# Kernel tuning notes

Hardware: AMD Instinct MI355X
Metric: run time of the kernel (lower is better)

## Reference

```python
import jax, jax.numpy as jnp
import numpy as np

H = 128
N_EXPERT = 100000
N_TEAM = 50000
N_EDGE = 600000
N_LABEL = 500000


def _sage(x_src, x_dst, src, dst, Wl, Wr, b, n_dst):
    # PyG SAGEConv: lin_l(mean of gathered neighbor feats) + lin_r(x_dst)
    msg = x_src[src]                                   # [E, H] gather
    agg = jax.ops.segment_sum(msg, dst, num_segments=n_dst)      # [n_dst, H]
    cnt = jax.ops.segment_sum(jnp.ones((src.shape[0], 1), x_src.dtype), dst,
                              num_segments=n_dst)      # [n_dst, 1]
    agg = agg / jnp.maximum(cnt, 1.0)
    return agg @ Wl + b + x_dst @ Wr


def setup_inputs() -> dict:
    key = jax.random.key(0)
    ks = jax.random.split(key, 20)
    inp = {
        'x_expert': jax.random.normal(ks[0], (N_EXPERT, H), jnp.float32),
        'x_team': jax.random.normal(ks[1], (N_TEAM, H), jnp.float32),
        'src_expert': jax.random.randint(ks[2], (N_EDGE,), 0, N_EXPERT),
        'dst_team': jax.random.randint(ks[3], (N_EDGE,), 0, N_TEAM),
        'label_src': jax.random.randint(ks[4], (N_LABEL,), 0, N_EXPERT),
        'label_dst': jax.random.randint(ks[5], (N_LABEL,), 0, N_TEAM),
    }
    s = 0.02
    names = ['W1et_l', 'W1et_r', 'W1te_l', 'W1te_r',
             'W2et_l', 'W2et_r', 'W2te_l', 'W2te_r']
    for i, n in enumerate(names):
        inp[n] = s * jax.random.normal(ks[6 + i], (H, H), jnp.float32)
    for i, n in enumerate(['b1et', 'b1te', 'b2et', 'b2te']):
        inp[n] = jnp.zeros((H,), jnp.float32)
    return inp


def reference(x_expert, x_team, src_expert, dst_team, label_src, label_dst,
              W1et_l, W1et_r, W1te_l, W1te_r,
              W2et_l, W2et_r, W2te_l, W2te_r,
              b1et, b1te, b2et, b2te):
    n_e, n_t = x_expert.shape[0], x_team.shape[0]
    # layer 1 (hetero: expert->team and reverse team->expert), ReLU
    h_team = jax.nn.relu(_sage(x_expert, x_team, src_expert, dst_team,
                               W1et_l, W1et_r, b1et, n_t))
    h_expert = jax.nn.relu(_sage(x_team, x_expert, dst_team, src_expert,
                                 W1te_l, W1te_r, b1te, n_e))
    # layer 2, no activation
    z_team = _sage(h_expert, h_team, src_expert, dst_team,
                   W2et_l, W2et_r, b2et, n_t)
    z_expert = _sage(h_team, h_expert, dst_team, src_expert,
                     W2te_l, W2te_r, b2te, n_e)
    # edge dot-product classifier on supervision edges
    return (z_expert[label_src] * z_team[label_dst]).sum(axis=-1)
```

## Files before the change

kernel.cpp:

```cpp
#include <hip/hip_runtime.h>

#define H 128
#define CH 4096
typedef unsigned short ushort_t;
typedef unsigned int uint_t;
typedef unsigned long long u64_t;
using s16x8 = __attribute__((ext_vector_type(8))) short;
using f32x4 = __attribute__((ext_vector_type(4))) float;
using h2 = __attribute__((ext_vector_type(2))) _Float16;

__device__ __forceinline__ float dot2(uint_t a, uint_t b, float c) {
  return __builtin_amdgcn_fdot2(__builtin_bit_cast(h2, a), __builtin_bit_cast(h2, b), c, false);
}
__device__ __forceinline__ uint_t pkh(float a, float b) {
  return __builtin_bit_cast(uint_t, __builtin_amdgcn_cvt_pkrtz(a, b));
}

__device__ __forceinline__ void gload_lds16(const void* g, void* l) {
  __builtin_amdgcn_global_load_lds(
      (const __attribute__((address_space(1))) unsigned int*)(unsigned long long)g,
      (__attribute__((address_space(3))) unsigned int*)(unsigned int)(unsigned long long)l,
      16, 0, 0);
}

__global__ __launch_bounds__(256) void prep_kernel(
    const float* __restrict__ xa, const float* __restrict__ xb,
    size_t n4a, size_t n4tot, uint2* __restrict__ xout,
    const float* __restrict__ Wl0, const float* __restrict__ Wr0,
    const float* __restrict__ Wl1, const float* __restrict__ Wr1,
    const float* __restrict__ Wl2, const float* __restrict__ Wr2,
    const float* __restrict__ Wl3, const float* __restrict__ Wr3,
    ushort_t* __restrict__ wdst, int* __restrict__ bcnt, int nbz) {
  const int b = blockIdx.x;
  const int tid = threadIdx.x;
  if (b < 2048) {
    size_t i = (size_t)b * 256 + tid;
    size_t s = 2048 * 256;
    for (; i < n4tot; i += s) {
      float4 v = (i < n4a) ? ((const float4*)xa)[i] : ((const float4*)xb)[i - n4a];
      uint2 r;
      r.x = pkh(v.x, v.y);
      r.y = pkh(v.z, v.w);
      xout[i] = r;
    }
  } else if (b < 2560) {
    int i = (b - 2048) * 256 + tid;
    int w = i >> 15;
    int ii = i & 32767;
    int j = ii & 7;
    int lane = (ii >> 3) & 63;
    int nf = (ii >> 9) & 7;
    int ks = ii >> 12;
    int k = ks * 32 + (lane >> 4) * 8 + j;
    int nn = nf * 16 + (lane & 15);
    const float* Wl = (w == 0) ? Wl0 : (w == 1) ? Wl1 : (w == 2) ? Wl2 : Wl3;
    const float* Wr = (w == 0) ? Wr0 : (w == 1) ? Wr1 : (w == 2) ? Wr2 : Wr3;
    float v = (k < H) ? Wl[k * H + nn] : Wr[(k - H) * H + nn];
    wdst[i] = __builtin_bit_cast(ushort_t, (_Float16)v);
  } else {
    for (int i = tid; i < nbz; i += 256) bcnt[i] = 0;
  }
}

__global__ __launch_bounds__(256) void bucket_count(
    const int* __restrict__ src, const int* __restrict__ dst, const int* __restrict__ ld,
    int* __restrict__ bcnt, int E, int L, int nct, int NBt, int NBe) {
  __shared__ int hist[256];
  const int b = blockIdx.x;
  const int tid = threadIdx.x;
  int stream, i0, n, base, shift;
  if (b < nct) { stream = 0; i0 = b * CH; n = E; base = 0; shift = 8; }
  else if (b < 2 * nct) { stream = 1; i0 = (b - nct) * CH; n = E; base = NBt; shift = 9; }
  else { stream = 2; i0 = (b - 2 * nct) * CH; n = L; base = NBt + NBe; shift = 8; }
  const int* idx = (stream == 0) ? dst : (stream == 1) ? src : ld;
  const int i1 = min(n, i0 + CH);
  hist[tid] = 0;
  __syncthreads();
  for (int i = i0 + tid; i < i1; i += 256) atomicAdd(&hist[idx[i] >> shift], 1);
  __syncthreads();
  int h = hist[tid];
  if (h) atomicAdd(&bcnt[base + tid], h);
}

__global__ void scan_buckets(const int* __restrict__ bcnt, int* __restrict__ boff,
                             int* __restrict__ cur, int n) {
  __shared__ int s[256];
  const int t = threadIdx.x;
  int carry = 0;
  for (int base = 0; base < n; base += 256) {
    int i = base + t;
    int v = (i < n) ? bcnt[i] : 0;
    s[t] = v;
    __syncthreads();
    for (int off = 1; off < 256; off <<= 1) {
      int x = (t >= off) ? s[t - off] : 0;
      __syncthreads();
      s[t] += x;
      __syncthreads();
    }
    if (i < n) { boff[i] = s[t] - v + carry; cur[i] = s[t] - v + carry; }
    __syncthreads();
    carry += s[255];
    __syncthreads();
  }
  if (t == 0) boff[n] = carry;
}

__global__ __launch_bounds__(256) void bucket_scatter(
    const int* __restrict__ src, const int* __restrict__ dst,
    const int* __restrict__ ls, const int* __restrict__ ld,
    int* __restrict__ cur, u64_t* __restrict__ recs,
    int E, int L, int nct, int NBt, int NBe) {
  __shared__ int hist[256];
  __shared__ int start[256];
  const int b = blockIdx.x;
  const int tid = threadIdx.x;
  int stream, i0, n, base;
  if (b < nct) { stream = 0; i0 = b * CH; n = E; base = 0; }
  else if (b < 2 * nct) { stream = 1; i0 = (b - nct) * CH; n = E; base = NBt; }
  else { stream = 2; i0 = (b - 2 * nct) * CH; n = L; base = NBt + NBe; }
  const int i1 = min(n, i0 + CH);

  hist[tid] = 0;
  __syncthreads();
  for (int i = i0 + tid; i < i1; i += 256) {
    int d = (stream == 0) ? dst[i] : (stream == 1) ? src[i] : ld[i];
    int bkt = (stream == 1) ? (d >> 9) : (d >> 8);
    atomicAdd(&hist[bkt], 1);
  }
  __syncthreads();
  int h = hist[tid];
  if (h) start[tid] = atomicAdd(&cur[base + tid], h);
  __syncthreads();
  for (int i = i0 + tid; i < i1; i += 256) {
    u64_t rec;
    int bkt;
    if (stream == 0) {
      int d = dst[i];
      rec = ((u64_t)d << 32) | (uint_t)src[i];
      bkt = d >> 8;
    } else if (stream == 1) {
      int d = src[i];
      rec = ((u64_t)d << 32) | (uint_t)dst[i];
      bkt = d >> 9;
    } else {
      int d = ld[i];
      rec = ((u64_t)d << 40) | ((u64_t)(uint_t)ls[i] << 20) | (uint_t)i;
      bkt = d >> 8;
    }
    int pos = start[bkt] + atomicSub(&hist[bkt], 1) - 1;
    recs[pos] = rec;
  }
}

__global__ __launch_bounds__(256) void place_all(
    const u64_t* __restrict__ recs, const int* __restrict__ boff,
    int* __restrict__ off_t, int* __restrict__ off_e, int* __restrict__ off_l,
    int* __restrict__ adj_t, int* __restrict__ adj_e_m, long long* __restrict__ lpair_m,
    int n_t, int n_e, int NBt, int NBe, int NBl) {
  __shared__ int sh[512];
  __shared__ int tmp[256];
  const int b = blockIdx.x;
  const int tid = threadIdx.x;
  int stream, d0, d1, nmax;
  int* offg;
  if (b < NBt) { stream = 0; d0 = b << 8; d1 = min(n_t, d0 + 256); offg = off_t; nmax = n_t; }
  else if (b < NBt + NBe) { stream = 1; d0 = (b - NBt) << 9; d1 = min(n_e, d0 + 512); offg = off_e; nmax = n_e; }
  else { stream = 2; d0 = (b - NBt - NBe) << 8; d1 = min(n_t, d0 + 256); offg = off_l; nmax = n_t; }
  const int nn = d1 - d0;
  const int rs = boff[b], re = boff[b + 1];

  sh[tid] = 0;
  sh[tid + 256] = 0;
  __syncthreads();
  for (int i = rs + tid; i < re; i += 256) {
    u64_t rec = recs[i];
    int d = (stream == 2) ? (int)(rec >> 40) : (int)(rec >> 32);
    atomicAdd(&sh[d - d0], 1);
  }
  __syncthreads();
  int carry = 0;
  for (int c = 0; c < 2; ++c) {
    int idx = c * 256 + tid;
    int v = sh[idx];
    tmp[tid] = v;
    __syncthreads();
    for (int o = 1; o < 256; o <<= 1) {
      int x = (tid >= o) ? tmp[tid - o] : 0;
      __syncthreads();
      tmp[tid] += x;
      __syncthreads();
    }
    int excl = tmp[tid] - v + carry;
    if (idx < nn) {
      offg[d0 + idx] = rs + excl;
      sh[idx] = rs + excl;
    }
    __syncthreads();
    carry += tmp[255];
    __syncthreads();
  }
  if (tid == 0) {
    bool last = (stream == 0 && b == NBt - 1) ||
                (stream == 1 && b == NBt + NBe - 1) ||
                (stream == 2 && b == NBt + NBe + NBl - 1);
    if (last) offg[nmax] = re;
  }
  __syncthreads();
  if (stream == 0) {
    for (int i = rs + tid; i < re; i += 256) {
      u64_t rec = recs[i];
      int d = (int)(rec >> 32);
      adj_t[atomicAdd(&sh[d - d0], 1)] = (int)rec;
    }
  } else if (stream == 1) {
    for (int i = rs + tid; i < re; i += 256) {
      u64_t rec = recs[i];
      int d = (int)(rec >> 32);
      adj_e_m[atomicAdd(&sh[d - d0], 1)] = (int)rec;
    }
  } else {
    for (int i = rs + tid; i < re; i += 256) {
      u64_t rec = recs[i];
      int d = (int)(rec >> 40);
      int lsv = (int)((rec >> 20) & 0xFFFFF);
      int li = (int)(rec & 0xFFFFF);
      lpair_m[atomicAdd(&sh[d - d0], 1)] = ((long long)lsv << 32) | (uint_t)li;
    }
  }
}

__global__ void pull_mean_dual(
    const ushort_t* __restrict__ featA, const int* __restrict__ offA, const int* __restrict__ adjA,
    ushort_t* __restrict__ outA, int nA,
    const ushort_t* __restrict__ featB, const int* __restrict__ offB, const int* __restrict__ adjB,
    ushort_t* __restrict__ outB, int nB) {
  int gid = blockIdx.x * blockDim.x + threadIdx.x;
  int wave = gid >> 6;
  int lane = gid & 63;
  int slot = lane >> 4;
  int sl = lane & 15;
  int nw = (gridDim.x * blockDim.x) >> 6;
  for (int v = wave; v < nA + nB; v += nw) {
    const uint4* f;
    const int* off;
    const int* adj;
    uint4* o;
    int vv;
    if (v < nA) {
      f = (const uint4*)featA; off = offA; adj = adjA; o = (uint4*)outA; vv = v;
    } else {
      f = (const uint4*)featB; off = offB; adj = adjB; o = (uint4*)outB; vv = v - nA;
    }
    int s = off[vv], e = off[vv + 1];
    float acc[8];
#pragma unroll
    for (int c = 0; c < 8; ++c) acc[c] = 0.f;
#pragma unroll 2
    for (int i = s; i < e; i += 4) {
      int j = i + slot;
      bool val = j < e;
      int idx = adj[val ? j : i];
      uint4 u = f[(size_t)idx * 16 + sl];
      uint_t s_lo = val ? 0x00003C00u : 0u;
      uint_t s_hi = val ? 0x3C000000u : 0u;
      acc[0] = dot2(u.x, s_lo, acc[0]); acc[1] = dot2(u.x, s_hi, acc[1]);
      acc[2] = dot2(u.y, s_lo, acc[2]); acc[3] = dot2(u.y, s_hi, acc[3]);
      acc[4] = dot2(u.z, s_lo, acc[4]); acc[5] = dot2(u.z, s_hi, acc[5]);
      acc[6] = dot2(u.w, s_lo, acc[6]); acc[7] = dot2(u.w, s_hi, acc[7]);
    }
#pragma unroll
    for (int c = 0; c < 8; ++c) {
      acc[c] += __shfl_xor(acc[c], 16);
      acc[c] += __shfl_xor(acc[c], 32);
    }
    if (slot == 0) {
      float rd = 1.0f / fmaxf((float)(e - s), 1.0f);
      uint4 ov;
      ov.x = pkh(acc[0] * rd, acc[1] * rd);
      ov.y = pkh(acc[2] * rd, acc[3] * rd);
      ov.z = pkh(acc[4] * rd, acc[5] * rd);
      ov.w = pkh(acc[6] * rd, acc[7] * rd);
      o[(size_t)vv * 16 + sl] = ov;
    }
  }
}

template <bool RELU>
__global__ __launch_bounds__(256, 2) void gemm_mfma_dual(
    const ushort_t* __restrict__ aggA, const ushort_t* __restrict__ xdA,
    const ushort_t* __restrict__ wfA, const float* __restrict__ biasA,
    ushort_t* __restrict__ outA, int nA, int gA,
    const ushort_t* __restrict__ aggB, const ushort_t* __restrict__ xdB,
    const ushort_t* __restrict__ wfB, const float* __restrict__ biasB,
    ushort_t* __restrict__ outB, int nB) {
  __shared__ __align__(16) ushort_t sA[64 * 128];
  __shared__ __align__(16) ushort_t sX[64 * 128];
  const ushort_t *agg, *xd, *wfrag;
  const float* bias;
  ushort_t* outp;
  int n, b0, nbl;
  if ((int)blockIdx.x < gA) {
    agg = aggA; xd = xdA; wfrag = wfA; bias = biasA; outp = outA; n = nA;
    b0 = blockIdx.x; nbl = gA;
  } else {
    agg = aggB; xd = xdB; wfrag = wfB; bias = biasB; outp = outB; n = nB;
    b0 = blockIdx.x - gA; nbl = gridDim.x - gA;
  }
  const int t = threadIdx.x;
  const int lane = t & 63;
  const int wid = t >> 6;
  const int mrow = (wid >> 1) * 32;
  const int nhalf = (wid & 1) * 64;

  s16x8 B[8][4];
#pragma unroll
  for (int ks = 0; ks < 8; ++ks)
#pragma unroll
    for (int nfi = 0; nfi < 4; ++nfi)
      B[ks][nfi] = *(const s16x8*)(wfrag + (size_t)(((ks << 3) | ((nhalf >> 4) + nfi)) << 9) + (lane << 3));

  float bv[4];
#pragma unroll
  for (int nfi = 0; nfi < 4; ++nfi) bv[nfi] = bias[nhalf + nfi * 16 + (lane & 15)];

  const int lrow = lane >> 4;
  const int pbyte = (lane & 15) << 4;

  const int ntiles = (n + 63) >> 6;
  for (int tile = b0; tile < ntiles; tile += nbl) {
    const int row0 = tile << 6;
#pragma unroll
    for (int i = 0; i < 8; ++i) {
      int reg = (wid << 3) + i;
      int rr = ((reg & 15) << 2) + lrow;
      int row = row0 + rr;
      row = row < n ? row : n - 1;
      int pp = pbyte ^ ((rr & 7) << 4);
      const ushort_t* srcp = (reg < 16 ? agg : xd) + (size_t)row * H + (pp >> 1);
      ushort_t* ldst = (reg < 16 ? sA : sX) + ((reg & 15) << 9);
      gload_lds16(srcp, ldst);
    }
    __syncthreads();

    f32x4 acc[2][4];
#pragma unroll
    for (int mi = 0; mi < 2; ++mi)
#pragma unroll
      for (int nfi = 0; nfi < 4; ++nfi) {
        f32x4 c = {bv[nfi], bv[nfi], bv[nfi], bv[nfi]};
        acc[mi][nfi] = c;
      }

    const int rr0 = mrow + (lane & 15);
    const int rr1 = rr0 + 16;
    const int kx = (lane >> 4) << 4;
    const int sw = (rr0 & 7) << 4;
#pragma unroll
    for (int ks = 0; ks < 8; ++ks) {
      const ushort_t* base = (ks < 4) ? sA : sX;
      const int kb = (ks & 3) << 6;
      s16x8 a0 = *(const s16x8*)((const char*)base + rr0 * 256 + ((kb | kx) ^ sw));
      s16x8 a1 = *(const s16x8*)((const char*)base + rr1 * 256 + ((kb | kx) ^ sw));
#pragma unroll
      for (int nfi = 0; nfi < 4; ++nfi) {
        acc[0][nfi] = __builtin_amdgcn_mfma_f32_16x16x32_f16(a0, B[ks][nfi], acc[0][nfi], 0, 0, 0);
        acc[1][nfi] = __builtin_amdgcn_mfma_f32_16x16x32_f16(a1, B[ks][nfi], acc[1][nfi], 0, 0, 0);
      }
    }

#pragma unroll
    for (int mi = 0; mi < 2; ++mi) {
      int rbase = row0 + mrow + mi * 16 + ((lane >> 4) << 2);
#pragma unroll
      for (int r = 0; r < 4; ++r) {
        int row = rbase + r;
        if (row < n) {
#pragma unroll
          for (int nfi = 0; nfi < 4; ++nfi) {
            float v = acc[mi][nfi][r];
            if (RELU) v = fmaxf(v, 0.f);
            outp[(size_t)row * H + nhalf + nfi * 16 + (lane & 15)] =
                __builtin_bit_cast(ushort_t, (_Float16)v);
          }
        }
      }
    }
    __syncthreads();
  }
}

__global__ void edge_dot_grouped(const ushort_t* __restrict__ ze, const ushort_t* __restrict__ zt,
                                 const int* __restrict__ loff, const long long* __restrict__ lpair,
                                 float* __restrict__ out, int n_t) {
  int gid = blockIdx.x * blockDim.x + threadIdx.x;
  int wave = gid >> 6;
  int lane = gid & 63;
  int slot = lane >> 4;
  int sl = lane & 15;
  int nw = (gridDim.x * blockDim.x) >> 6;
  const uint4* fz = (const uint4*)ze;
  const uint4* ft = (const uint4*)zt;
  for (int v = wave; v < n_t; v += nw) {
    int s = loff[v], e = loff[v + 1];
    if (s == e) continue;
    uint4 b = ft[(size_t)v * 16 + sl];
    for (int i = s; i < e; i += 4) {
      int j = i + slot;
      bool val = j < e;
      long long q = lpair[val ? j : i];
      int row = (int)(q >> 32);
      uint4 u = fz[(size_t)row * 16 + sl];
      float p = dot2(u.x, b.x, dot2(u.y, b.y, dot2(u.z, b.z, dot2(u.w, b.w, 0.f))));
      p += __shfl_xor(p, 1);
      p += __shfl_xor(p, 2);
      p += __shfl_xor(p, 4);
      p += __shfl_xor(p, 8);
      if (sl == 0 && val) __builtin_nontemporal_store(p, &out[(int)q]);
    }
  }
}

extern "C" void kernel_launch(void* const* d_in, const int* in_sizes, int n_in,
                              void* d_out, int out_size, void* d_ws, size_t ws_size,
                              hipStream_t stream) {
  const float* x_e = (const float*)d_in[0];
  const float* x_t = (const float*)d_in[1];
  const int* src = (const int*)d_in[2];
  const int* dst = (const int*)d_in[3];
  const int* ls = (const int*)d_in[4];
  const int* ld = (const int*)d_in[5];
  const float* W1et_l = (const float*)d_in[6];
  const float* W1et_r = (const float*)d_in[7];
  const float* W1te_l = (const float*)d_in[8];
  const float* W1te_r = (const float*)d_in[9];
  const float* W2et_l = (const float*)d_in[10];
  const float* W2et_r = (const float*)d_in[11];
  const float* W2te_l = (const float*)d_in[12];
  const float* W2te_r = (const float*)d_in[13];
  const float* b1et = (const float*)d_in[14];
  const float* b1te = (const float*)d_in[15];
  const float* b2et = (const float*)d_in[16];
  const float* b2te = (const float*)d_in[17];

  const int n_e = in_sizes[0] / H;
  const int n_t = in_sizes[1] / H;
  const int E = in_sizes[2];
  const int L = in_sizes[4];
  float* out = (float*)d_out;

  const size_t fe = (size_t)n_e * H;
  const size_t ft = (size_t)n_t * H;
  ushort_t* us = (ushort_t*)d_ws;
  ushort_t* xb_e = us;
  ushort_t* xb_t = xb_e + fe;
  ushort_t* agg_e = xb_t + ft;
  ushort_t* agg_t = agg_e + fe;
  ushort_t* h_e = agg_t + ft;
  ushort_t* h_t = h_e + fe;
  ushort_t* wfrag = h_t + ft;
  int* ib = (int*)(wfrag + 4 * 32768);

  const int Mt = n_t + 1, Me = n_e + 1, Ml = n_t + 1;
  const int NBt = (n_t + 255) >> 8;
  const int NBe = (n_e + 511) >> 9;
  const int NBl = NBt;
  const int NBtot = NBt + NBe + NBl;

  int* off = ib;
  int* bcnt = off + Mt + Me + Ml;
  int* boff = bcnt + NBtot + 1;
  int* cur = boff + NBtot + 1;
  int* adj_t = cur + NBtot;
  int* adj_e = adj_t + E;
  long long* lpair = (long long*)(((unsigned long long)(adj_e + E) + 7) & ~7ULL);
  u64_t* recs = (u64_t*)(lpair + L);

  int* off_t = off;
  int* off_e = off + Mt;
  int* off_l = off + Mt + Me;
  int* adj_e_m = adj_e - E;
  long long* lpair_m = lpair - 2 * (size_t)E;

  const int nct = (E + CH - 1) / CH;
  const int ncl = (L + CH - 1) / CH;

  const dim3 blk(256);

  prep_kernel<<<2561, blk, 0, stream>>>(x_e, x_t, fe / 4, (fe + ft) / 4, (uint2*)xb_e,
                                        W1et_l, W1et_r, W1te_l, W1te_r,
                                        W2et_l, W2et_r, W2te_l, W2te_r,
                                        wfrag, bcnt, NBtot + 1);

  bucket_count<<<2 * nct + ncl, blk, 0, stream>>>(src, dst, ld, bcnt, E, L, nct, NBt, NBe);
  scan_buckets<<<1, blk, 0, stream>>>(bcnt, boff, cur, NBtot);
  bucket_scatter<<<2 * nct + ncl, blk, 0, stream>>>(src, dst, ls, ld, cur, recs,
                                                    E, L, nct, NBt, NBe);
  place_all<<<NBtot, blk, 0, stream>>>(recs, boff, off_t, off_e, off_l,
                                       adj_t, adj_e_m, lpair_m, n_t, n_e, NBt, NBe, NBl);

  const int gt = (n_t + 63) / 64, ge = (n_e + 63) / 64;
  const int gA = min(gt, 512), gB = min(ge, 512);
  const int npull = ((n_t + n_e) + 3) / 4;

  pull_mean_dual<<<npull, blk, 0, stream>>>(xb_e, off_t, adj_t, agg_t, n_t,
                                            xb_t, off_e, adj_e_m, agg_e, n_e);
  gemm_mfma_dual<true><<<gA + gB, blk, 0, stream>>>(
      agg_t, xb_t, wfrag + 0 * 32768, b1et, h_t, n_t, gA,
      agg_e, xb_e, wfrag + 1 * 32768, b1te, h_e, n_e);

  pull_mean_dual<<<npull, blk, 0, stream>>>(h_e, off_t, adj_t, agg_t, n_t,
                                            h_t, off_e, adj_e_m, agg_e, n_e);
  gemm_mfma_dual<false><<<gA + gB, blk, 0, stream>>>(
      agg_t, h_t, wfrag + 2 * 32768, b2et, agg_t, n_t, gA,
      agg_e, h_e, wfrag + 3 * 32768, b2te, agg_e, n_e);

  edge_dot_grouped<<<(n_t + 3) / 4, blk, 0, stream>>>(agg_e, agg_t, off_l, lpair_m, out, n_t);
}
```

Measured before the change: 250.7 us.

## Fuse bucket counting into prep, regroup labels by expert, vectorize adjacency reads

The bucket histogram pass is folded into the prep kernel as extra blocks, and the zeroing of bucket counters moves to a memset. This removes one kernel launch. Supervision edges are now grouped by expert (label_src) instead of team, so each wave holds an expert row and gathers team rows, which come from a smaller table. The pull-mean and edge-dot loops now give each 16-lane slot four consecutive edges, with int4 loads of adjacency indices. That can leave lanes idle on low-degree nodes, and the int4 loads may be unaligned.

```diff
diff --git a/kernel.cpp b/kernel.cpp
--- a/kernel.cpp
+++ b/kernel.cpp
@@ -15,6 +15,8 @@
 __device__ __forceinline__ uint_t pkh(float a, float b) {
   return __builtin_bit_cast(uint_t, __builtin_amdgcn_cvt_pkrtz(a, b));
 }
+#define LO1 0x00003C00u
+#define HI1 0x3C000000u
 
 __device__ __forceinline__ void gload_lds16(const void* g, void* l) {
   __builtin_amdgcn_global_load_lds(
@@ -30,7 +32,9 @@
     const float* __restrict__ Wl1, const float* __restrict__ Wr1,
     const float* __restrict__ Wl2, const float* __restrict__ Wr2,
     const float* __restrict__ Wl3, const float* __restrict__ Wr3,
-    ushort_t* __restrict__ wdst, int* __restrict__ bcnt, int nbz) {
+    ushort_t* __restrict__ wdst,
+    const int* __restrict__ src, const int* __restrict__ dst, const int* __restrict__ ls,
+    int* __restrict__ bcnt, int E, int L, int nct, int NBt, int NBe) {
   const int b = blockIdx.x;
   const int tid = threadIdx.x;
   if (b < 2048) {
@@ -58,28 +62,21 @@
     float v = (k < H) ? Wl[k * H + nn] : Wr[(k - H) * H + nn];
     wdst[i] = __builtin_bit_cast(ushort_t, (_Float16)v);
   } else {
-    for (int i = tid; i < nbz; i += 256) bcnt[i] = 0;
-  }
-}
-
-__global__ __launch_bounds__(256) void bucket_count(
-    const int* __restrict__ src, const int* __restrict__ dst, const int* __restrict__ ld,
-    int* __restrict__ bcnt, int E, int L, int nct, int NBt, int NBe) {
-  __shared__ int hist[256];
-  const int b = blockIdx.x;
-  const int tid = threadIdx.x;
-  int stream, i0, n, base, shift;
-  if (b < nct) { stream = 0; i0 = b * CH; n = E; base = 0; shift = 8; }
-  else if (b < 2 * nct) { stream = 1; i0 = (b - nct) * CH; n = E; base = NBt; shift = 9; }
-  else { stream = 2; i0 = (b - 2 * nct) * CH; n = L; base = NBt + NBe; shift = 8; }
-  const int* idx = (stream == 0) ? dst : (stream == 1) ? src : ld;
-  const int i1 = min(n, i0 + CH);
-  hist[tid] = 0;
-  __syncthreads();
-  for (int i = i0 + tid; i < i1; i += 256) atomicAdd(&hist[idx[i] >> shift], 1);
-  __syncthreads();
-  int h = hist[tid];
-  if (h) atomicAdd(&bcnt[base + tid], h);
+    __shared__ int hist[256];
+    int cb = b - 2560;
+    int stream, i0, n, base, shift;
+    if (cb < nct) { stream = 0; i0 = cb * CH; n = E; base = 0; shift = 8; }
+    else if (cb < 2 * nct) { stream = 1; i0 = (cb - nct) * CH; n = E; base = NBt; shift = 9; }
+    else { stream = 2; i0 = (cb - 2 * nct) * CH; n = L; base = NBt + NBe; shift = 9; }
+    const int* idx = (stream == 0) ? dst : (stream == 1) ? src : ls;
+    const int i1 = min(n, i0 + CH);
+    hist[tid] = 0;
+    __syncthreads();
+    for (int i = i0 + tid; i < i1; i += 256) atomicAdd(&hist[idx[i] >> shift], 1);
+    __syncthreads();
+    int h = hist[tid];
+    if (h) atomicAdd(&bcnt[base + tid], h);
+  }
 }
 
 __global__ void scan_buckets(const int* __restrict__ bcnt, int* __restrict__ boff,
@@ -124,8 +121,8 @@
   hist[tid] = 0;
   __syncthreads();
   for (int i = i0 + tid; i < i1; i += 256) {
-    int d = (stream == 0) ? dst[i] : (stream == 1) ? src[i] : ld[i];
-    int bkt = (stream == 1) ? (d >> 9) : (d >> 8);
+    int d = (stream == 0) ? dst[i] : (stream == 1) ? src[i] : ls[i];
+    int bkt = (stream == 0) ? (d >> 8) : (d >> 9);
     atomicAdd(&hist[bkt], 1);
   }
   __syncthreads();
@@ -144,9 +141,9 @@
       rec = ((u64_t)d << 32) | (uint_t)dst[i];
       bkt = d >> 9;
     } else {
-      int d = ld[i];
-      rec = ((u64_t)d << 40) | ((u64_t)(uint_t)ls[i] << 20) | (uint_t)i;
-      bkt = d >> 8;
+      int d = ls[i];
+      rec = ((u64_t)d << 40) | ((u64_t)(uint_t)ld[i] << 20) | (uint_t)i;
+      bkt = d >> 9;
     }
     int pos = start[bkt] + atomicSub(&hist[bkt], 1) - 1;
     recs[pos] = rec;
@@ -157,7 +154,7 @@
     const u64_t* __restrict__ recs, const int* __restrict__ boff,
     int* __restrict__ off_t, int* __restrict__ off_e, int* __restrict__ off_l,
     int* __restrict__ adj_t, int* __restrict__ adj_e_m, long long* __restrict__ lpair_m,
-    int n_t, int n_e, int NBt, int NBe, int NBl) {
+    int n_t, int n_e, int NBt, int NBe) {
   __shared__ int sh[512];
   __shared__ int tmp[256];
   const int b = blockIdx.x;
@@ -166,7 +163,7 @@
   int* offg;
   if (b < NBt) { stream = 0; d0 = b << 8; d1 = min(n_t, d0 + 256); offg = off_t; nmax = n_t; }
   else if (b < NBt + NBe) { stream = 1; d0 = (b - NBt) << 9; d1 = min(n_e, d0 + 512); offg = off_e; nmax = n_e; }
-  else { stream = 2; d0 = (b - NBt - NBe) << 8; d1 = min(n_t, d0 + 256); offg = off_l; nmax = n_t; }
+  else { stream = 2; d0 = (b - NBt - NBe) << 9; d1 = min(n_e, d0 + 512); offg = off_l; nmax = n_e; }
   const int nn = d1 - d0;
   const int rs = boff[b], re = boff[b + 1];
 
@@ -203,7 +200,7 @@
   if (tid == 0) {
     bool last = (stream == 0 && b == NBt - 1) ||
                 (stream == 1 && b == NBt + NBe - 1) ||
-                (stream == 2 && b == NBt + NBe + NBl - 1);
+                (stream == 2 && b == NBt + NBe + NBe - 1);
     if (last) offg[nmax] = re;
   }
   __syncthreads();
@@ -223,9 +220,9 @@
     for (int i = rs + tid; i < re; i += 256) {
       u64_t rec = recs[i];
       int d = (int)(rec >> 40);
-      int lsv = (int)((rec >> 20) & 0xFFFFF);
+      int ldv = (int)((rec >> 20) & 0xFFFFF);
       int li = (int)(rec & 0xFFFFF);
-      lpair_m[atomicAdd(&sh[d - d0], 1)] = ((long long)lsv << 32) | (uint_t)li;
+      lpair_m[atomicAdd(&sh[d - d0], 1)] = ((long long)ldv << 32) | (uint_t)li;
     }
   }
 }
@@ -256,18 +253,22 @@
     float acc[8];
 #pragma unroll
     for (int c = 0; c < 8; ++c) acc[c] = 0.f;
-#pragma unroll 2
-    for (int i = s; i < e; i += 4) {
-      int j = i + slot;
-      bool val = j < e;
-      int idx = adj[val ? j : i];
-      uint4 u = f[(size_t)idx * 16 + sl];
-      uint_t s_lo = val ? 0x00003C00u : 0u;
-      uint_t s_hi = val ? 0x3C000000u : 0u;
-      acc[0] = dot2(u.x, s_lo, acc[0]); acc[1] = dot2(u.x, s_hi, acc[1]);
-      acc[2] = dot2(u.y, s_lo, acc[2]); acc[3] = dot2(u.y, s_hi, acc[3]);
-      acc[4] = dot2(u.z, s_lo, acc[4]); acc[5] = dot2(u.z, s_hi, acc[5]);
-      acc[6] = dot2(u.w, s_lo, acc[6]); acc[7] = dot2(u.w, s_hi, acc[7]);
+    for (int i = s; i < e; i += 16) {
+      int j0 = i + 4 * slot;
+      if (j0 < e) {
+        int4 a4 = *(const int4*)&adj[j0];
+#pragma unroll
+        for (int k = 0; k < 4; ++k) {
+          if (j0 + k < e) {
+            int idx = (k == 0) ? a4.x : (k == 1) ? a4.y : (k == 2) ? a4.z : a4.w;
+            uint4 u = f[(size_t)idx * 16 + sl];
+            acc[0] = dot2(u.x, LO1, acc[0]); acc[1] = dot2(u.x, HI1, acc[1]);
+            acc[2] = dot2(u.y, LO1, acc[2]); acc[3] = dot2(u.y, HI1, acc[3]);
+            acc[4] = dot2(u.z, LO1, acc[4]); acc[5] = dot2(u.z, HI1, acc[5]);
+            acc[6] = dot2(u.w, LO1, acc[6]); acc[7] = dot2(u.w, HI1, acc[7]);
+          }
+        }
+      }
     }
 #pragma unroll
     for (int c = 0; c < 8; ++c) {
@@ -390,33 +391,40 @@
   }
 }
 
-__global__ void edge_dot_grouped(const ushort_t* __restrict__ ze, const ushort_t* __restrict__ zt,
+__global__ void edge_dot_grouped(const ushort_t* __restrict__ zheld, const ushort_t* __restrict__ zgath,
                                  const int* __restrict__ loff, const long long* __restrict__ lpair,
-                                 float* __restrict__ out, int n_t) {
+                                 float* __restrict__ out, int nheld) {
   int gid = blockIdx.x * blockDim.x + threadIdx.x;
   int wave = gid >> 6;
   int lane = gid & 63;
   int slot = lane >> 4;
   int sl = lane & 15;
   int nw = (gridDim.x * blockDim.x) >> 6;
-  const uint4* fz = (const uint4*)ze;
-  const uint4* ft = (const uint4*)zt;
-  for (int v = wave; v < n_t; v += nw) {
+  const uint4* fh = (const uint4*)zheld;
+  const uint4* fg = (const uint4*)zgath;
+  for (int v = wave; v < nheld; v += nw) {
     int s = loff[v], e = loff[v + 1];
     if (s == e) continue;
-    uint4 b = ft[(size_t)v * 16 + sl];
-    for (int i = s; i < e; i += 4) {
-      int j = i + slot;
-      bool val = j < e;
-      long long q = lpair[val ? j : i];
-      int row = (int)(q >> 32);
-      uint4 u = fz[(size_t)row * 16 + sl];
-      float p = dot2(u.x, b.x, dot2(u.y, b.y, dot2(u.z, b.z, dot2(u.w, b.w, 0.f))));
-      p += __shfl_xor(p, 1);
-      p += __shfl_xor(p, 2);
-      p += __shfl_xor(p, 4);
-      p += __shfl_xor(p, 8);
-      if (sl == 0 && val) __builtin_nontemporal_store(p, &out[(int)q]);
+    uint4 b = fh[(size_t)v * 16 + sl];
+    for (int i = s; i < e; i += 16) {
+      int j0 = i + 4 * slot;
+      if (j0 < e) {
+#pragma unroll
+        for (int k = 0; k < 4; ++k) {
+          int j = j0 + k;
+          if (j < e) {
+            long long q = lpair[j];
+            int row = (int)(q >> 32);
+            uint4 u = fg[(size_t)row * 16 + sl];
+            float p = dot2(u.x, b.x, dot2(u.y, b.y, dot2(u.z, b.z, dot2(u.w, b.w, 0.f))));
+            p += __shfl_xor(p, 1);
+            p += __shfl_xor(p, 2);
+            p += __shfl_xor(p, 4);
+            p += __shfl_xor(p, 8);
+            if (sl == 0) __builtin_nontemporal_store(p, &out[(int)q]);
+          }
+        }
+      }
     }
   }
 }
@@ -461,14 +469,13 @@
   ushort_t* wfrag = h_t + ft;
   int* ib = (int*)(wfrag + 4 * 32768);
 
-  const int Mt = n_t + 1, Me = n_e + 1, Ml = n_t + 1;
+  const int Mt = n_t + 1, Me = n_e + 1;
   const int NBt = (n_t + 255) >> 8;
   const int NBe = (n_e + 511) >> 9;
-  const int NBl = NBt;
-  const int NBtot = NBt + NBe + NBl;
+  const int NBtot = NBt + NBe + NBe;
 
   int* off = ib;
-  int* bcnt = off + Mt + Me + Ml;
+  int* bcnt = off + Mt + Me + Me;
   int* boff = bcnt + NBtot + 1;
   int* cur = boff + NBtot + 1;
   int* adj_t = cur + NBtot;
@@ -484,20 +491,20 @@
 
   const int nct = (E + CH - 1) / CH;
   const int ncl = (L + CH - 1) / CH;
+  const int nbc = 2 * nct + ncl;
 
   const dim3 blk(256);
 
-  prep_kernel<<<2561, blk, 0, stream>>>(x_e, x_t, fe / 4, (fe + ft) / 4, (uint2*)xb_e,
-                                        W1et_l, W1et_r, W1te_l, W1te_r,
-                                        W2et_l, W2et_r, W2te_l, W2te_r,
-                                        wfrag, bcnt, NBtot + 1);
-
-  bucket_count<<<2 * nct + ncl, blk, 0, stream>>>(src, dst, ld, bcnt, E, L, nct, NBt, NBe);
+  hipMemsetAsync(bcnt, 0, (size_t)(NBtot + 1) * 4, stream);
+  prep_kernel<<<2560 + nbc, blk, 0, stream>>>(
+      x_e, x_t, fe / 4, (fe + ft) / 4, (uint2*)xb_e,
+      W1et_l, W1et_r, W1te_l, W1te_r, W2et_l, W2et_r, W2te_l, W2te_r, wfrag,
+      src, dst, ls, bcnt, E, L, nct, NBt, NBe);
+
   scan_buckets<<<1, blk, 0, stream>>>(bcnt, boff, cur, NBtot);
-  bucket_scatter<<<2 * nct + ncl, blk, 0, stream>>>(src, dst, ls, ld, cur, recs,
-                                                    E, L, nct, NBt, NBe);
+  bucket_scatter<<<nbc, blk, 0, stream>>>(src, dst, ls, ld, cur, recs, E, L, nct, NBt, NBe);
   place_all<<<NBtot, blk, 0, stream>>>(recs, boff, off_t, off_e, off_l,
-                                       adj_t, adj_e_m, lpair_m, n_t, n_e, NBt, NBe, NBl);
+                                       adj_t, adj_e_m, lpair_m, n_t, n_e, NBt, NBe);
 
   const int gt = (n_t + 63) / 64, ge = (n_e + 63) / 64;
   const int gA = min(gt, 512), gB = min(ge, 512);
@@ -515,5 +522,5 @@
       agg_t, h_t, wfrag + 2 * 32768, b2et, agg_t, n_t, gA,
       agg_e, h_e, wfrag + 3 * 32768, b2te, agg_e, n_e);
 
-  edge_dot_grouped<<<(n_t + 3) / 4, blk, 0, stream>>>(agg_e, agg_t, off_l, lpair_m, out, n_t);
-}
+  edge_dot_grouped<<<(n_e + 3) / 4, blk, 0, stream>>>(agg_e, agg_t, off_l, lpair_m, out, n_e);
+}
```

Measured after the change: 306.8 us. 22.4% more time.
